# Kernel tuning notes

Hardware: AMD Instinct MI355X
Metric: run time of the kernel (lower is better)

Reference implementation:

```python
import math
import jax, jax.numpy as jnp
import numpy as np

B, W_LEN, C = 4, 2048, 768
H = 3  # fixed number of heads in the module
K = C // H  # head dim


def setup_inputs() -> dict:
    key = jax.random.key(0)
    k1, k2, k3 = jax.random.split(key, 3)
    in_sequence_bwc = jax.random.normal(k1, (B, W_LEN, C), dtype=jnp.float32)
    # torch nn.Linear weights: [out_features, in_features], scaled for stability
    W_qkv = jax.random.normal(k2, (3 * C, C), dtype=jnp.float32) * (1.0 / math.sqrt(C))
    W_proj = jax.random.normal(k3, (C, C), dtype=jnp.float32) * (1.0 / math.sqrt(C))
    return {"in_sequence_bwc": in_sequence_bwc, "W_qkv": W_qkv, "W_proj": W_proj}


def reference(in_sequence_bwc, W_qkv, W_proj):
    batch, words, coords = in_sequence_bwc.shape
    head_dim = coords // H
    # qkv projection: x @ W^T  -> [b, w, 3c]
    all_bwd = jnp.einsum("bwc,dc->bwd", in_sequence_bwc, W_qkv)
    q_bwc, k_bwc, v_bwc = jnp.split(all_bwd, 3, axis=-1)
    # [b, h, w, k]
    q = q_bwc.reshape(batch, words, H, head_dim).transpose(0, 2, 1, 3)
    k = k_bwc.reshape(batch, words, H, head_dim).transpose(0, 2, 1, 3)
    v = v_bwc.reshape(batch, words, H, head_dim).transpose(0, 2, 1, 3)
    # scaled scores with causal mask -> softmax -> @V
    scores = jnp.einsum("bhqk,bhmk->bhqm", q, k) / math.sqrt(head_dim)
    causal = jnp.tril(jnp.ones((words, words), dtype=bool))
    scores = jnp.where(causal[None, None], scores, -jnp.inf)
    probs = jax.nn.softmax(scores, axis=-1)
    out = jnp.einsum("bhqm,bhmk->bhqk", probs, v)
    out_bwc = out.transpose(0, 2, 1, 3).reshape(batch, words, coords)
    return jnp.einsum("bwc,dc->bwd", out_bwc, W_proj)
```

## Files before the change

### kernel.cpp

```cpp
#include <hip/hip_runtime.h>

using v8h = __attribute__((ext_vector_type(8))) _Float16;
using v4f = __attribute__((ext_vector_type(4))) float;
using v4u = __attribute__((ext_vector_type(4))) unsigned short;
using v8u = __attribute__((ext_vector_type(8))) unsigned short;

__device__ __forceinline__ unsigned short f2h(float x) {
  _Float16 h = (_Float16)x;
  return __builtin_bit_cast(unsigned short, h);
}
__device__ __forceinline__ float h2f(unsigned short u) {
  return (float)__builtin_bit_cast(_Float16, u);
}

__device__ __forceinline__ void gl_lds16(const unsigned short* g, unsigned short* l) {
  __builtin_amdgcn_global_load_lds(
      (const __attribute__((address_space(1))) unsigned int*)g,
      (__attribute__((address_space(3))) unsigned int*)l, 16, 0, 0);
}

__global__ void cvt3_kernel(const float* __restrict__ X,
                            const float* __restrict__ Wq,
                            const float* __restrict__ Wp,
                            unsigned short* __restrict__ Xb,
                            unsigned short* __restrict__ Wqb,
                            unsigned short* __restrict__ Wpb) {
  const int blk = (int)blockIdx.x;
  const float* src;
  unsigned short* dst;
  int i;
  if (blk < 3072)      { src = X;  dst = Xb;  i = blk * 256 + threadIdx.x; }
  else if (blk < 3936) { src = Wq; dst = Wqb; i = (blk - 3072) * 256 + threadIdx.x; }
  else                 { src = Wp; dst = Wpb; i = (blk - 3936) * 256 + threadIdx.x; }
  const float* p = src + (size_t)i * 8;
  float4 a = *(const float4*)p;
  float4 b = *(const float4*)(p + 4);
  v8u o = {f2h(a.x), f2h(a.y), f2h(a.z), f2h(a.w),
           f2h(b.x), f2h(b.y), f2h(b.z), f2h(b.w)};
  *(v8u*)(dst + (size_t)i * 8) = o;
}

template <int OMODE>
__global__ __launch_bounds__(512, 2)
void gemm8_kernel(const unsigned short* __restrict__ A,
                  const unsigned short* __restrict__ Bw,
                  void* __restrict__ Cout) {
  __shared__ unsigned short sm[65536];
  const int t    = (int)threadIdx.x;
  const int ln   = t & 63;
  const int wv   = t >> 6;
  const int quad = ln >> 4;
  const int L    = ln & 15;
  const int wm   = wv >> 2;
  const int wn   = wv & 3;
  const long m0  = (long)blockIdx.y * 256;
  const long n0  = (long)blockIdx.x * 256;

  const int srow = t >> 3;
  const int scol = ((t & 7) ^ (srow & 7)) * 8;
  const unsigned short* Ath = A + (m0 + srow) * 768 + scol;
  const unsigned short* Bth = Bw + (n0 + srow) * 768 + scol;
  unsigned short* lth = &sm[t * 8];

  const int l7   = L & 7;
  const int sl0  = ((0 + quad) ^ l7) * 8;
  const int sl1  = ((4 + quad) ^ l7) * 8;
  const int arow = (wm * 128 + L) * 64;
  const int brow = (wn * 64 + L) * 64;

  v4f acc[8][4];
#pragma unroll
  for (int i = 0; i < 8; i++)
#pragma unroll
    for (int j = 0; j < 4; j++) acc[i][j] = (v4f){0.f, 0.f, 0.f, 0.f};

  auto stA = [&](int tile, int h) {
    if (tile >= 12) return;
    const unsigned short* g = Ath + (h * 128) * 768 + tile * 64;
    unsigned short* l = lth + (tile & 1) * 32768 + h * 8192;
    gl_lds16(g, l);
    gl_lds16(g + 64 * 768, l + 4096);
  };
  auto stB = [&](int tile, int h) {
    if (tile >= 12) return;
    const unsigned short* g = Bth + (h * 128) * 768 + tile * 64;
    unsigned short* l = lth + (tile & 1) * 32768 + 16384 + h * 8192;
    gl_lds16(g, l);
    gl_lds16(g + 64 * 768, l + 4096);
  };

  stB(0, 0); stB(0, 1); stA(0, 0); stA(0, 1);
  stB(1, 0); stB(1, 1); stA(1, 0);
  asm volatile("s_waitcnt vmcnt(6)" ::: "memory");
  __builtin_amdgcn_s_barrier();
  __builtin_amdgcn_sched_barrier(0);

#pragma unroll 2
  for (int kt = 0; kt < 12; ++kt) {
    const unsigned short* sA = &sm[(kt & 1) * 32768];
    const unsigned short* sB = sA + 16384;
    v8h af[4][2], b0[2][2], b1[2][2];

#pragma unroll
    for (int i = 0; i < 4; i++) {
      af[i][0] = *(const v8h*)&sA[arow + i * 1024 + sl0];
      af[i][1] = *(const v8h*)&sA[arow + i * 1024 + sl1];
    }
#pragma unroll
    for (int j = 0; j < 2; j++) {
      b0[j][0] = *(const v8h*)&sB[brow + j * 1024 + sl0];
      b0[j][1] = *(const v8h*)&sB[brow + j * 1024 + sl1];
    }
    stA(kt + 1, 1);
    __builtin_amdgcn_s_barrier();
    asm volatile("s_waitcnt lgkmcnt(0)" ::: "memory");
    __builtin_amdgcn_sched_barrier(0);
    __builtin_amdgcn_s_setprio(1);
#pragma unroll
    for (int i = 0; i < 4; i++)
#pragma unroll
      for (int j = 0; j < 2; j++) {
        acc[i][j] = __builtin_amdgcn_mfma_f32_16x16x32_f16(af[i][0], b0[j][0], acc[i][j], 0, 0, 0);
        acc[i][j] = __builtin_amdgcn_mfma_f32_16x16x32_f16(af[i][1], b0[j][1], acc[i][j], 0, 0, 0);
      }
    __builtin_amdgcn_s_setprio(0);
    __builtin_amdgcn_s_barrier();
    __builtin_amdgcn_sched_barrier(0);

#pragma unroll
    for (int j = 0; j < 2; j++) {
      b1[j][0] = *(const v8h*)&sB[brow + 2048 + j * 1024 + sl0];
      b1[j][1] = *(const v8h*)&sB[brow + 2048 + j * 1024 + sl1];
    }
    __builtin_amdgcn_s_barrier();
    asm volatile("s_waitcnt lgkmcnt(0)" ::: "memory");
    __builtin_amdgcn_sched_barrier(0);
    __builtin_amdgcn_s_setprio(1);
#pragma unroll
    for (int i = 0; i < 4; i++)
#pragma unroll
      for (int j = 0; j < 2; j++) {
        acc[i][2 + j] = __builtin_amdgcn_mfma_f32_16x16x32_f16(af[i][0], b1[j][0], acc[i][2 + j], 0, 0, 0);
        acc[i][2 + j] = __builtin_amdgcn_mfma_f32_16x16x32_f16(af[i][1], b1[j][1], acc[i][2 + j], 0, 0, 0);
      }
    __builtin_amdgcn_s_setprio(0);
    __builtin_amdgcn_s_barrier();
    __builtin_amdgcn_sched_barrier(0);

#pragma unroll
    for (int i = 0; i < 4; i++) {
      af[i][0] = *(const v8h*)&sA[arow + 4096 + i * 1024 + sl0];
      af[i][1] = *(const v8h*)&sA[arow + 4096 + i * 1024 + sl1];
    }
    stB(kt + 2, 0);
    __builtin_amdgcn_s_barrier();
    asm volatile("s_waitcnt lgkmcnt(0)" ::: "memory");
    __builtin_amdgcn_sched_barrier(0);
    __builtin_amdgcn_s_setprio(1);
#pragma unroll
    for (int i = 0; i < 4; i++)
#pragma unroll
      for (int j = 0; j < 2; j++) {
        acc[4 + i][2 + j] = __builtin_amdgcn_mfma_f32_16x16x32_f16(af[i][0], b1[j][0], acc[4 + i][2 + j], 0, 0, 0);
        acc[4 + i][2 + j] = __builtin_amdgcn_mfma_f32_16x16x32_f16(af[i][1], b1[j][1], acc[4 + i][2 + j], 0, 0, 0);
      }
    __builtin_amdgcn_s_setprio(0);
    __builtin_amdgcn_s_barrier();
    __builtin_amdgcn_sched_barrier(0);

    stB(kt + 2, 1);
    stA(kt + 2, 0);
    __builtin_amdgcn_s_barrier();
    __builtin_amdgcn_sched_barrier(0);
    __builtin_amdgcn_s_setprio(1);
#pragma unroll
    for (int i = 0; i < 4; i++)
#pragma unroll
      for (int j = 0; j < 2; j++) {
        acc[4 + i][j] = __builtin_amdgcn_mfma_f32_16x16x32_f16(af[i][0], b0[j][0], acc[4 + i][j], 0, 0, 0);
        acc[4 + i][j] = __builtin_amdgcn_mfma_f32_16x16x32_f16(af[i][1], b0[j][1], acc[4 + i][j], 0, 0, 0);
      }
    __builtin_amdgcn_s_setprio(0);
    if (kt + 2 < 12)      { asm volatile("s_waitcnt vmcnt(6)" ::: "memory"); }
    else if (kt + 1 < 12) { asm volatile("s_waitcnt vmcnt(0)" ::: "memory"); }
    __builtin_amdgcn_s_barrier();
    __builtin_amdgcn_sched_barrier(0);
  }

#pragma unroll
  for (int mi = 0; mi < 8; mi++) {
    const long row = m0 + wm * 128 + (mi >> 2) * 64 + (mi & 3) * 16 + quad * 4;
#pragma unroll
    for (int nj = 0; nj < 4; nj++) {
      const long col = n0 + wn * 64 + nj * 16 + L;
#pragma unroll
      for (int r = 0; r < 4; r++) {
        if (OMODE == 0)
          ((unsigned short*)Cout)[(row + r) * 1536 + col] = f2h(acc[mi][nj][r]);
        else
          ((float*)Cout)[(row + r) * 768 + col] = acc[mi][nj][r];
      }
    }
  }
}

__global__ __launch_bounds__(512, 2)
void scv8_kernel(const unsigned short* __restrict__ QK,
                 const unsigned short* __restrict__ Xb,
                 const unsigned short* __restrict__ Wq,
                 unsigned short* __restrict__ Sc,
                 unsigned short* __restrict__ VT) {
  __shared__ unsigned short sm[65536];
  const int t    = (int)threadIdx.x;
  const int ln   = t & 63;
  const int wv   = t >> 6;
  const int quad = ln >> 4;
  const int L    = ln & 15;
  const int wm   = wv >> 2;
  const int wn   = wv & 3;

  const int x = (int)blockIdx.x;
  const bool isV = (x < 96);
  int NT, Ihi = 0, Jhi = 0, bh = 0, mt = 0, nt = 0;
  const unsigned short* Abase;
  const unsigned short* Bbase;
  long astr, bstr;

  if (isV) {
    mt = x & 31;
    nt = x >> 5;
    Abase = Xb + (long)mt * 256 * 768;
    Bbase = Wq + (long)(1536 + nt * 256) * 768;
    astr = 768; bstr = 768; NT = 12;
  } else {
    int s = x - 96;
    bh = s / 36;
    int slot = s % 36;
    while (slot >= Ihi + 1) { slot -= Ihi + 1; Ihi++; }
    Jhi = slot;
    const int b = bh / 3, h = bh % 3;
    Abase = QK + ((long)b * 2048 + Ihi * 256) * 1536 + h * 256;
    Bbase = QK + ((long)b * 2048 + Jhi * 256) * 1536 + 768 + h * 256;
    astr = 1536; bstr = 1536; NT = 4;
  }

  const int srow = t >> 3;
  const int scol = ((t & 7) ^ (srow & 7)) * 8;
  const unsigned short* Ath = Abase + (long)srow * astr + scol;
  const unsigned short* Bth = Bbase + (long)srow * bstr + scol;
  unsigned short* lth = &sm[t * 8];

  const int l7   = L & 7;
  const int sl0  = ((0 + quad) ^ l7) * 8;
  const int sl1  = ((4 + quad) ^ l7) * 8;
  const int arow = (wm * 128 + L) * 64;
  const int brow = (wn * 64 + L) * 64;

  v4f acc[8][4];
#pragma unroll
  for (int i = 0; i < 8; i++)
#pragma unroll
    for (int j = 0; j < 4; j++) acc[i][j] = (v4f){0.f, 0.f, 0.f, 0.f};

  auto stA = [&](int tile, int h) {
    if (tile >= NT) return;
    const unsigned short* g = Ath + (long)(h * 128) * astr + tile * 64;
    unsigned short* l = lth + (tile & 1) * 32768 + h * 8192;
    gl_lds16(g, l);
    gl_lds16(g + 64 * astr, l + 4096);
  };
  auto stB = [&](int tile, int h) {
    if (tile >= NT) return;
    const unsigned short* g = Bth + (long)(h * 128) * bstr + tile * 64;
    unsigned short* l = lth + (tile & 1) * 32768 + 16384 + h * 8192;
    gl_lds16(g, l);
    gl_lds16(g + 64 * bstr, l + 4096);
  };

  stB(0, 0); stB(0, 1); stA(0, 0); stA(0, 1);
  stB(1, 0); stB(1, 1); stA(1, 0);
  asm volatile("s_waitcnt vmcnt(6)" ::: "memory");
  __builtin_amdgcn_s_barrier();
  __builtin_amdgcn_sched_barrier(0);

#pragma unroll 2
  for (int kt = 0; kt < NT; ++kt) {
    const unsigned short* sA = &sm[(kt & 1) * 32768];
    const unsigned short* sB = sA + 16384;
    v8h af[4][2], b0[2][2], b1[2][2];

#pragma unroll
    for (int i = 0; i < 4; i++) {
      af[i][0] = *(const v8h*)&sA[arow + i * 1024 + sl0];
      af[i][1] = *(const v8h*)&sA[arow + i * 1024 + sl1];
    }
#pragma unroll
    for (int j = 0; j < 2; j++) {
      b0[j][0] = *(const v8h*)&sB[brow + j * 1024 + sl0];
      b0[j][1] = *(const v8h*)&sB[brow + j * 1024 + sl1];
    }
    stA(kt + 1, 1);
    __builtin_amdgcn_s_barrier();
    asm volatile("s_waitcnt lgkmcnt(0)" ::: "memory");
    __builtin_amdgcn_sched_barrier(0);
    __builtin_amdgcn_s_setprio(1);
#pragma unroll
    for (int i = 0; i < 4; i++)
#pragma unroll
      for (int j = 0; j < 2; j++) {
        acc[i][j] = __builtin_amdgcn_mfma_f32_16x16x32_f16(af[i][0], b0[j][0], acc[i][j], 0, 0, 0);
        acc[i][j] = __builtin_amdgcn_mfma_f32_16x16x32_f16(af[i][1], b0[j][1], acc[i][j], 0, 0, 0);
      }
    __builtin_amdgcn_s_setprio(0);
    __builtin_amdgcn_s_barrier();
    __builtin_amdgcn_sched_barrier(0);

#pragma unroll
    for (int j = 0; j < 2; j++) {
      b1[j][0] = *(const v8h*)&sB[brow + 2048 + j * 1024 + sl0];
      b1[j][1] = *(const v8h*)&sB[brow + 2048 + j * 1024 + sl1];
    }
    __builtin_amdgcn_s_barrier();
    asm volatile("s_waitcnt lgkmcnt(0)" ::: "memory");
    __builtin_amdgcn_sched_barrier(0);
    __builtin_amdgcn_s_setprio(1);
#pragma unroll
    for (int i = 0; i < 4; i++)
#pragma unroll
      for (int j = 0; j < 2; j++) {
        acc[i][2 + j] = __builtin_amdgcn_mfma_f32_16x16x32_f16(af[i][0], b1[j][0], acc[i][2 + j], 0, 0, 0);
        acc[i][2 + j] = __builtin_amdgcn_mfma_f32_16x16x32_f16(af[i][1], b1[j][1], acc[i][2 + j], 0, 0, 0);
      }
    __builtin_amdgcn_s_setprio(0);
    __builtin_amdgcn_s_barrier();
    __builtin_amdgcn_sched_barrier(0);

#pragma unroll
    for (int i = 0; i < 4; i++) {
      af[i][0] = *(const v8h*)&sA[arow + 4096 + i * 1024 + sl0];
      af[i][1] = *(const v8h*)&sA[arow + 4096 + i * 1024 + sl1];
    }
    stB(kt + 2, 0);
    __builtin_amdgcn_s_barrier();
    asm volatile("s_waitcnt lgkmcnt(0)" ::: "memory");
    __builtin_amdgcn_sched_barrier(0);
    __builtin_amdgcn_s_setprio(1);
#pragma unroll
    for (int i = 0; i < 4; i++)
#pragma unroll
      for (int j = 0; j < 2; j++) {
        acc[4 + i][2 + j] = __builtin_amdgcn_mfma_f32_16x16x32_f16(af[i][0], b1[j][0], acc[4 + i][2 + j], 0, 0, 0);
        acc[4 + i][2 + j] = __builtin_amdgcn_mfma_f32_16x16x32_f16(af[i][1], b1[j][1], acc[4 + i][2 + j], 0, 0, 0);
      }
    __builtin_amdgcn_s_setprio(0);
    __builtin_amdgcn_s_barrier();
    __builtin_amdgcn_sched_barrier(0);

    stB(kt + 2, 1);
    stA(kt + 2, 0);
    __builtin_amdgcn_s_barrier();
    __builtin_amdgcn_sched_barrier(0);
    __builtin_amdgcn_s_setprio(1);
#pragma unroll
    for (int i = 0; i < 4; i++)
#pragma unroll
      for (int j = 0; j < 2; j++) {
        acc[4 + i][j] = __builtin_amdgcn_mfma_f32_16x16x32_f16(af[i][0], b0[j][0], acc[4 + i][j], 0, 0, 0);
        acc[4 + i][j] = __builtin_amdgcn_mfma_f32_16x16x32_f16(af[i][1], b0[j][1], acc[4 + i][j], 0, 0, 0);
      }
    __builtin_amdgcn_s_setprio(0);
    if (kt + 2 < NT)      { asm volatile("s_waitcnt vmcnt(6)" ::: "memory"); }
    else if (kt + 1 < NT) { asm volatile("s_waitcnt vmcnt(0)" ::: "memory"); }
    __builtin_amdgcn_s_barrier();
    __builtin_amdgcn_sched_barrier(0);
  }

  if (isV) {
#pragma unroll
    for (int mi = 0; mi < 8; mi++) {
      const long token = (long)mt * 256 + wm * 128 + (mi >> 2) * 64 + (mi & 3) * 16 + quad * 4;
      const int b  = (int)(token >> 11);
      const int tk = (int)(token & 2047);
#pragma unroll
      for (int nj = 0; nj < 4; nj++) {
        const int colp = nt * 256 + wn * 64 + nj * 16 + L;
        const int h    = colp >> 8;
        const int d    = colp & 255;
        v4u val = {f2h(acc[mi][nj][0]), f2h(acc[mi][nj][1]),
                   f2h(acc[mi][nj][2]), f2h(acc[mi][nj][3])};
        *(v4u*)(&VT[((long)(b * 3 + h) * 256 + d) * 2048 + tk]) = val;
      }
    }
  } else {
    const int di = wm;
    const int dj = wn >> 1;
    const int i128 = 2 * Ihi + di;
    const int j128 = 2 * Jhi + dj;
    if (j128 <= i128) {
      unsigned short* Sb = Sc + ((long)bh * 136 + (long)i128 * (i128 + 1) / 2 + j128) * 16384;
#pragma unroll
      for (int mi = 0; mi < 8; mi++) {
        const int subrow = (mi >> 2) * 64 + (mi & 3) * 16 + quad * 4;
#pragma unroll
        for (int nj = 0; nj < 4; nj++) {
          const int subcol = (wn & 1) * 64 + nj * 16 + L;
#pragma unroll
          for (int r = 0; r < 4; r++)
            Sb[(subrow + r) * 128 + subcol] = f2h(acc[mi][nj][r]);
        }
      }
    }
  }
}

__global__ __launch_bounds__(512, 1)
void pvf_kernel(const unsigned short* __restrict__ Sc,
                const unsigned short* __restrict__ VT,
                unsigned short* __restrict__ AO) {
  __shared__ unsigned short sm[36864];
  __shared__ float fbuf[128];

  const int t    = (int)threadIdx.x;
  const int ln   = t & 63;
  const int wv   = t >> 6;
  const int quad = ln >> 4;
  const int L    = ln & 15;

  const int p  = (int)blockIdx.x >> 1;
  const int nh = (int)blockIdx.x & 1;
  const int bh = (int)blockIdx.y;
  const int b  = bh / 3, h = bh % 3;

  const unsigned short* VTb = VT + ((long)(bh * 256 + nh * 128)) * 2048;
  const int rloc = wv * 16 + L;

  auto stageV = [&](int jj, unsigned short* base) {
#pragma unroll
    for (int pp = 0; pp < 4; pp++) {
      const int sidx = pp * 512 + t;
      const int d    = sidx >> 4;
      const int ph   = sidx & 15;
      gl_lds16(VTb + (long)d * 2048 + jj * 128 + ((ph ^ (d & 7)) * 8),
               base + sidx * 8);
    }
  };

  for (int sel = 0; sel < 2; ++sel) {
    const int i = sel ? (15 - p) : p;
    const long Sbase = ((long)bh * 136 + (long)i * (i + 1) / 2) * 16384;

    v4f acc[8];
#pragma unroll
    for (int n = 0; n < 8; n++) acc[n] = (v4f){0.f, 0.f, 0.f, 0.f};
    float m_run = -1e30f, l_run = 0.f;

    v8u s_cur[4], s_nxt[4];
    {
      const unsigned short* Sp = Sc + Sbase + (long)rloc * 128;
#pragma unroll
      for (int ks = 0; ks < 4; ks++)
        s_cur[ks] = *(const v8u*)(Sp + ks * 32 + quad * 8);
      __builtin_amdgcn_sched_barrier(0);
      stageV(0, &sm[0]);
      __builtin_amdgcn_sched_barrier(0);
    }

    for (int j = 0; j <= i; ++j) {
      const int jn = (j < i) ? (j + 1) : i;
      const bool clamped = (j == i);
      {
        const unsigned short* Sp = Sc + Sbase + (long)jn * 16384 + (long)rloc * 128;
#pragma unroll
        for (int ks = 0; ks < 4; ks++)
          s_nxt[ks] = *(const v8u*)(Sp + ks * 32 + quad * 8);
      }
      __builtin_amdgcn_sched_barrier(0);
      if (clamped) {
#pragma unroll
        for (int pp = 0; pp < 4; pp++) {
          const int sidx = pp * 512 + t;
          const int d    = sidx >> 4;
          const int ph   = sidx & 15;
          gl_lds16(VTb + (long)d * 2048 + jn * 128 + ((ph ^ (d & 7)) * 8),
                   &sm[32768 + t * 8]);
        }
      } else {
        stageV(jn, &sm[(jn & 1) * 16384]);
      }
      __builtin_amdgcn_sched_barrier(0);

      float pv[4][8];
      float mx = -1e30f;
      if (j == i) {
#pragma unroll
        for (int ks = 0; ks < 4; ks++)
#pragma unroll
          for (int e = 0; e < 8; e++) {
            const bool valid = (ks * 32 + quad * 8 + e) <= rloc;
            const float f = valid ? h2f(s_cur[ks][e]) * 0.0625f : -1e30f;
            pv[ks][e] = f;
            mx = fmaxf(mx, f);
          }
      } else {
#pragma unroll
        for (int ks = 0; ks < 4; ks++)
#pragma unroll
          for (int e = 0; e < 8; e++) {
            const float f = h2f(s_cur[ks][e]) * 0.0625f;
            pv[ks][e] = f;
            mx = fmaxf(mx, f);
          }
      }
      mx = fmaxf(mx, __shfl_xor(mx, 16));
      mx = fmaxf(mx, __shfl_xor(mx, 32));
      const float m_new = fmaxf(m_run, mx);
      const float alpha = __expf(m_run - m_new);
      m_run = m_new;

      float sum = 0.f;
      v8h pa[4];
#pragma unroll
      for (int ks = 0; ks < 4; ks++) {
        v8h ph16;
#pragma unroll
        for (int e = 0; e < 8; e++) {
          const float pe = __expf(pv[ks][e] - m_new);
          sum += pe;
          ph16[e] = (_Float16)pe;
        }
        pa[ks] = ph16;
      }
      sum += __shfl_xor(sum, 16);
      sum += __shfl_xor(sum, 32);
      l_run = l_run * alpha + sum;

      if (quad == 0) fbuf[wv * 16 + L] = alpha;
      asm volatile("s_waitcnt lgkmcnt(0)" ::: "memory");
      __builtin_amdgcn_sched_barrier(0);
      const float a0 = fbuf[wv * 16 + quad * 4 + 0];
      const float a1 = fbuf[wv * 16 + quad * 4 + 1];
      const float a2 = fbuf[wv * 16 + quad * 4 + 2];
      const float a3 = fbuf[wv * 16 + quad * 4 + 3];
#pragma unroll
      for (int n = 0; n < 8; n++) {
        acc[n][0] *= a0; acc[n][1] *= a1; acc[n][2] *= a2; acc[n][3] *= a3;
      }

      asm volatile("s_waitcnt vmcnt(8)" ::: "memory");
      __builtin_amdgcn_s_barrier();
      __builtin_amdgcn_sched_barrier(0);

      const unsigned short* vb = &sm[(j & 1) * 16384];
      const int dx = L & 7;
#pragma unroll
      for (int nfc = 0; nfc < 8; nfc++) {
        const int dbase = (nfc * 16 + L) * 128;
        v8h v0 = *(const v8h*)&vb[dbase + ((0 + quad) ^ dx) * 8];
        v8h v1 = *(const v8h*)&vb[dbase + ((4 + quad) ^ dx) * 8];
        v8h v2 = *(const v8h*)&vb[dbase + ((8 + quad) ^ dx) * 8];
        v8h v3 = *(const v8h*)&vb[dbase + ((12 + quad) ^ dx) * 8];
        acc[nfc] = __builtin_amdgcn_mfma_f32_16x16x32_f16(pa[0], v0, acc[nfc], 0, 0, 0);
        acc[nfc] = __builtin_amdgcn_mfma_f32_16x16x32_f16(pa[1], v1, acc[nfc], 0, 0, 0);
        acc[nfc] = __builtin_amdgcn_mfma_f32_16x16x32_f16(pa[2], v2, acc[nfc], 0, 0, 0);
        acc[nfc] = __builtin_amdgcn_mfma_f32_16x16x32_f16(pa[3], v3, acc[nfc], 0, 0, 0);
      }
      __builtin_amdgcn_s_barrier();
      __builtin_amdgcn_sched_barrier(0);

#pragma unroll
      for (int ks = 0; ks < 4; ks++) s_cur[ks] = s_nxt[ks];
    }

    const float inv = 1.0f / l_run;
    if (quad == 0) fbuf[wv * 16 + L] = inv;
    asm volatile("s_waitcnt lgkmcnt(0)" ::: "memory");
    __builtin_amdgcn_sched_barrier(0);
    const float i0 = fbuf[wv * 16 + quad * 4 + 0];
    const float i1 = fbuf[wv * 16 + quad * 4 + 1];
    const float i2 = fbuf[wv * 16 + quad * 4 + 2];
    const float i3 = fbuf[wv * 16 + quad * 4 + 3];

    unsigned short* Ob = AO + ((long)b * 2048 + (long)i * 128 + wv * 16 + quad * 4) * 768
                            + h * 256 + nh * 128 + L;
#pragma unroll
    for (int n = 0; n < 8; n++) {
      Ob[0 * 768 + n * 16] = f2h(acc[n][0] * i0);
      Ob[1 * 768 + n * 16] = f2h(acc[n][1] * i1);
      Ob[2 * 768 + n * 16] = f2h(acc[n][2] * i2);
      Ob[3 * 768 + n * 16] = f2h(acc[n][3] * i3);
    }
    __builtin_amdgcn_s_barrier();
  }
}

extern "C" void kernel_launch(void* const* d_in, const int* in_sizes, int n_in,
                              void* d_out, int out_size, void* d_ws, size_t ws_size,
                              hipStream_t stream) {
  const float* X     = (const float*)d_in[0];
  const float* Wqkv  = (const float*)d_in[1];
  const float* Wproj = (const float*)d_in[2];
  float* out = (float*)d_out;

  const size_t SZ_QK = (size_t)8192 * 1536 * 2;
  const size_t SZ_VT = (size_t)3072 * 2048 * 2;
  const size_t SZ_SC = (size_t)12 * 136 * 16384 * 2;
  const size_t SZ_AO = (size_t)8192 * 768 * 2;
  const size_t SZ_WQ = (size_t)2304 * 768 * 2;

  char* ws = (char*)d_ws;
  unsigned short* QKb = (unsigned short*)ws;
  unsigned short* VTb = (unsigned short*)(ws + SZ_QK);
  unsigned short* Scb = (unsigned short*)(ws + SZ_QK + SZ_VT);
  unsigned short* AOb = (unsigned short*)(ws + SZ_QK + SZ_VT + SZ_SC);
  unsigned short* Xb  = AOb;
  unsigned short* Wqb = (unsigned short*)(ws + SZ_QK + SZ_VT + SZ_SC + SZ_AO);
  unsigned short* Wpb = (unsigned short*)(ws + SZ_QK + SZ_VT + SZ_SC + SZ_AO + SZ_WQ);

  dim3 blk(256, 1, 1);
  cvt3_kernel<<<dim3(4224, 1, 1), blk, 0, stream>>>(X, Wqkv, Wproj, Xb, Wqb, Wpb);
  gemm8_kernel<0><<<dim3(6, 32, 1), dim3(512, 1, 1), 0, stream>>>(Xb, Wqb, QKb);
  scv8_kernel<<<dim3(528, 1, 1), dim3(512, 1, 1), 0, stream>>>(QKb, Xb, Wqb, Scb, VTb);
  pvf_kernel<<<dim3(16, 12, 1), dim3(512, 1, 1), 0, stream>>>(Scb, VTb, AOb);
  gemm8_kernel<1><<<dim3(3, 32, 1), dim3(512, 1, 1), 0, stream>>>(AOb, Wpb, out);
}
```

Measured before the change: 227.6 us.

## Load V fragments directly from global into registers in PV kernel

Drops the LDS double-buffered staging of the V tile, the swizzled gl_lds loads and both workgroup barriers per iteration in the PV kernel. Each lane now loads its V fragments straight from global/L2 into registers. The softmax probabilities are recomputed from the raw scores instead of being kept in a float array. The aim is to cut barrier syncs and LDS traffic, at the cost of redundant global reads across the 8 waves, higher register pressure, and exposed load latency because the V loads are no longer prefetched one step ahead.

```diff
diff --git a/kernel.cpp b/kernel.cpp
--- a/kernel.cpp
+++ b/kernel.cpp
@@ -417,7 +417,6 @@
 void pvf_kernel(const unsigned short* __restrict__ Sc,
                 const unsigned short* __restrict__ VT,
                 unsigned short* __restrict__ AO) {
-  __shared__ unsigned short sm[36864];
   __shared__ float fbuf[128];
 
   const int t    = (int)threadIdx.x;
@@ -434,16 +433,7 @@
   const unsigned short* VTb = VT + ((long)(bh * 256 + nh * 128)) * 2048;
   const int rloc = wv * 16 + L;
 
-  auto stageV = [&](int jj, unsigned short* base) {
-#pragma unroll
-    for (int pp = 0; pp < 4; pp++) {
-      const int sidx = pp * 512 + t;
-      const int d    = sidx >> 4;
-      const int ph   = sidx & 15;
-      gl_lds16(VTb + (long)d * 2048 + jj * 128 + ((ph ^ (d & 7)) * 8),
-               base + sidx * 8);
-    }
-  };
+  const unsigned short* Vl = VTb + (long)L * 2048 + quad * 8;
 
   for (int sel = 0; sel < 2; ++sel) {
     const int i = sel ? (15 - p) : p;
@@ -460,36 +450,23 @@
 #pragma unroll
       for (int ks = 0; ks < 4; ks++)
         s_cur[ks] = *(const v8u*)(Sp + ks * 32 + quad * 8);
-      __builtin_amdgcn_sched_barrier(0);
-      stageV(0, &sm[0]);
-      __builtin_amdgcn_sched_barrier(0);
     }
 
     for (int j = 0; j <= i; ++j) {
       const int jn = (j < i) ? (j + 1) : i;
-      const bool clamped = (j == i);
       {
         const unsigned short* Sp = Sc + Sbase + (long)jn * 16384 + (long)rloc * 128;
 #pragma unroll
         for (int ks = 0; ks < 4; ks++)
           s_nxt[ks] = *(const v8u*)(Sp + ks * 32 + quad * 8);
       }
-      __builtin_amdgcn_sched_barrier(0);
-      if (clamped) {
-#pragma unroll
-        for (int pp = 0; pp < 4; pp++) {
-          const int sidx = pp * 512 + t;
-          const int d    = sidx >> 4;
-          const int ph   = sidx & 15;
-          gl_lds16(VTb + (long)d * 2048 + jn * 128 + ((ph ^ (d & 7)) * 8),
-                   &sm[32768 + t * 8]);
-        }
-      } else {
-        stageV(jn, &sm[(jn & 1) * 16384]);
-      }
-      __builtin_amdgcn_sched_barrier(0);
-
-      float pv[4][8];
+      v8h vf[4][8];
+#pragma unroll
+      for (int ks = 0; ks < 4; ks++)
+#pragma unroll
+        for (int nfc = 0; nfc < 8; nfc++)
+          vf[ks][nfc] = *(const v8h*)(Vl + (long)nfc * 32768 + j * 128 + ks * 32);
+
       float mx = -1e30f;
       if (j == i) {
 #pragma unroll
@@ -498,18 +475,14 @@
           for (int e = 0; e < 8; e++) {
             const bool valid = (ks * 32 + quad * 8 + e) <= rloc;
             const float f = valid ? h2f(s_cur[ks][e]) * 0.0625f : -1e30f;
-            pv[ks][e] = f;
             mx = fmaxf(mx, f);
           }
       } else {
 #pragma unroll
         for (int ks = 0; ks < 4; ks++)
 #pragma unroll
-          for (int e = 0; e < 8; e++) {
-            const float f = h2f(s_cur[ks][e]) * 0.0625f;
-            pv[ks][e] = f;
-            mx = fmaxf(mx, f);
-          }
+          for (int e = 0; e < 8; e++)
+            mx = fmaxf(mx, h2f(s_cur[ks][e]) * 0.0625f);
       }
       mx = fmaxf(mx, __shfl_xor(mx, 16));
       mx = fmaxf(mx, __shfl_xor(mx, 32));
@@ -519,16 +492,32 @@
 
       float sum = 0.f;
       v8h pa[4];
-#pragma unroll
-      for (int ks = 0; ks < 4; ks++) {
-        v8h ph16;
-#pragma unroll
-        for (int e = 0; e < 8; e++) {
-          const float pe = __expf(pv[ks][e] - m_new);
-          sum += pe;
-          ph16[e] = (_Float16)pe;
+      if (j == i) {
+#pragma unroll
+        for (int ks = 0; ks < 4; ks++) {
+          v8h ph16;
+#pragma unroll
+          for (int e = 0; e < 8; e++) {
+            const bool valid = (ks * 32 + quad * 8 + e) <= rloc;
+            const float f = valid ? h2f(s_cur[ks][e]) * 0.0625f : -1e30f;
+            const float pe = __expf(f - m_new);
+            sum += pe;
+            ph16[e] = (_Float16)pe;
+          }
+          pa[ks] = ph16;
         }
-        pa[ks] = ph16;
+      } else {
+#pragma unroll
+        for (int ks = 0; ks < 4; ks++) {
+          v8h ph16;
+#pragma unroll
+          for (int e = 0; e < 8; e++) {
+            const float pe = __expf(h2f(s_cur[ks][e]) * 0.0625f - m_new);
+            sum += pe;
+            ph16[e] = (_Float16)pe;
+          }
+          pa[ks] = ph16;
+        }
       }
       sum += __shfl_xor(sum, 16);
       sum += __shfl_xor(sum, 32);
@@ -541,31 +530,20 @@
       const float a1 = fbuf[wv * 16 + quad * 4 + 1];
       const float a2 = fbuf[wv * 16 + quad * 4 + 2];
       const float a3 = fbuf[wv * 16 + quad * 4 + 3];
+      asm volatile("s_waitcnt lgkmcnt(0)" ::: "memory");
+      __builtin_amdgcn_sched_barrier(0);
 #pragma unroll
       for (int n = 0; n < 8; n++) {
         acc[n][0] *= a0; acc[n][1] *= a1; acc[n][2] *= a2; acc[n][3] *= a3;
       }
 
-      asm volatile("s_waitcnt vmcnt(8)" ::: "memory");
-      __builtin_amdgcn_s_barrier();
-      __builtin_amdgcn_sched_barrier(0);
-
-      const unsigned short* vb = &sm[(j & 1) * 16384];
-      const int dx = L & 7;
 #pragma unroll
       for (int nfc = 0; nfc < 8; nfc++) {
-        const int dbase = (nfc * 16 + L) * 128;
-        v8h v0 = *(const v8h*)&vb[dbase + ((0 + quad) ^ dx) * 8];
-        v8h v1 = *(const v8h*)&vb[dbase + ((4 + quad) ^ dx) * 8];
-        v8h v2 = *(const v8h*)&vb[dbase + ((8 + quad) ^ dx) * 8];
-        v8h v3 = *(const v8h*)&vb[dbase + ((12 + quad) ^ dx) * 8];
-        acc[nfc] = __builtin_amdgcn_mfma_f32_16x16x32_f16(pa[0], v0, acc[nfc], 0, 0, 0);
-        acc[nfc] = __builtin_amdgcn_mfma_f32_16x16x32_f16(pa[1], v1, acc[nfc], 0, 0, 0);
-        acc[nfc] = __builtin_amdgcn_mfma_f32_16x16x32_f16(pa[2], v2, acc[nfc], 0, 0, 0);
-        acc[nfc] = __builtin_amdgcn_mfma_f32_16x16x32_f16(pa[3], v3, acc[nfc], 0, 0, 0);
-      }
-      __builtin_amdgcn_s_barrier();
-      __builtin_amdgcn_sched_barrier(0);
+        acc[nfc] = __builtin_amdgcn_mfma_f32_16x16x32_f16(pa[0], vf[0][nfc], acc[nfc], 0, 0, 0);
+        acc[nfc] = __builtin_amdgcn_mfma_f32_16x16x32_f16(pa[1], vf[1][nfc], acc[nfc], 0, 0, 0);
+        acc[nfc] = __builtin_amdgcn_mfma_f32_16x16x32_f16(pa[2], vf[2][nfc], acc[nfc], 0, 0, 0);
+        acc[nfc] = __builtin_amdgcn_mfma_f32_16x16x32_f16(pa[3], vf[3][nfc], acc[nfc], 0, 0, 0);
+      }
 
 #pragma unroll
       for (int ks = 0; ks < 4; ks++) s_cur[ks] = s_nxt[ks];
@@ -579,6 +557,8 @@
     const float i1 = fbuf[wv * 16 + quad * 4 + 1];
     const float i2 = fbuf[wv * 16 + quad * 4 + 2];
     const float i3 = fbuf[wv * 16 + quad * 4 + 3];
+    asm volatile("s_waitcnt lgkmcnt(0)" ::: "memory");
+    __builtin_amdgcn_sched_barrier(0);
 
     unsigned short* Ob = AO + ((long)b * 2048 + (long)i * 128 + wv * 16 + quad * 4) * 768
                             + h * 256 + nh * 128 + L;
@@ -589,7 +569,6 @@
       Ob[2 * 768 + n * 16] = f2h(acc[n][2] * i2);
       Ob[3 * 768 + n * 16] = f2h(acc[n][3] * i3);
     }
-    __builtin_amdgcn_s_barrier();
   }
 }
 
```

New measurement: 317.9 us. 1.4x slower.

## Split paired causal row tiles into separate blocks and raise PV kernel occupancy

Applied to the files above, without the earlier changes.

The PV/softmax kernel previously processed two complementary causal row tiles per block. Each block now handles a single row tile, with the grid doubled and longest tiles scheduled first, so more CUs get work. Launch bounds now target four blocks per CU, and the LDS buffer drops the extra clamp slot by skipping the prefetch on the last iteration. The tighter register budget may cause spills, and per-block load balance is left to the hardware scheduler.

```diff
diff --git a/kernel.cpp b/kernel.cpp
--- a/kernel.cpp
+++ b/kernel.cpp
@@ -413,11 +413,11 @@
   }
 }
 
-__global__ __launch_bounds__(512, 1)
+__global__ __launch_bounds__(512, 4)
 void pvf_kernel(const unsigned short* __restrict__ Sc,
                 const unsigned short* __restrict__ VT,
                 unsigned short* __restrict__ AO) {
-  __shared__ unsigned short sm[36864];
+  __shared__ unsigned short sm[32768];
   __shared__ float fbuf[128];
 
   const int t    = (int)threadIdx.x;
@@ -426,8 +426,9 @@
   const int quad = ln >> 4;
   const int L    = ln & 15;
 
-  const int p  = (int)blockIdx.x >> 1;
-  const int nh = (int)blockIdx.x & 1;
+  const int x  = (int)blockIdx.x;
+  const int i  = 15 - (x >> 1);
+  const int nh = x & 1;
   const int bh = (int)blockIdx.y;
   const int b  = bh / 3, h = bh % 3;
 
@@ -445,151 +446,136 @@
     }
   };
 
-  for (int sel = 0; sel < 2; ++sel) {
-    const int i = sel ? (15 - p) : p;
-    const long Sbase = ((long)bh * 136 + (long)i * (i + 1) / 2) * 16384;
-
-    v4f acc[8];
-#pragma unroll
-    for (int n = 0; n < 8; n++) acc[n] = (v4f){0.f, 0.f, 0.f, 0.f};
-    float m_run = -1e30f, l_run = 0.f;
-
-    v8u s_cur[4], s_nxt[4];
-    {
-      const unsigned short* Sp = Sc + Sbase + (long)rloc * 128;
+  const long Sbase = ((long)bh * 136 + (long)i * (i + 1) / 2) * 16384;
+
+  v4f acc[8];
+#pragma unroll
+  for (int n = 0; n < 8; n++) acc[n] = (v4f){0.f, 0.f, 0.f, 0.f};
+  float m_run = -1e30f, l_run = 0.f;
+
+  v8u s_cur[4], s_nxt[4];
+  {
+    const unsigned short* Sp = Sc + Sbase + (long)rloc * 128;
+#pragma unroll
+    for (int ks = 0; ks < 4; ks++)
+      s_cur[ks] = *(const v8u*)(Sp + ks * 32 + quad * 8);
+    __builtin_amdgcn_sched_barrier(0);
+    stageV(0, &sm[0]);
+    __builtin_amdgcn_sched_barrier(0);
+  }
+
+  for (int j = 0; j <= i; ++j) {
+    const bool last = (j == i);
+    if (!last) {
+      const unsigned short* Sp = Sc + Sbase + (long)(j + 1) * 16384 + (long)rloc * 128;
 #pragma unroll
       for (int ks = 0; ks < 4; ks++)
-        s_cur[ks] = *(const v8u*)(Sp + ks * 32 + quad * 8);
+        s_nxt[ks] = *(const v8u*)(Sp + ks * 32 + quad * 8);
       __builtin_amdgcn_sched_barrier(0);
-      stageV(0, &sm[0]);
+      stageV(j + 1, &sm[((j + 1) & 1) * 16384]);
       __builtin_amdgcn_sched_barrier(0);
     }
 
-    for (int j = 0; j <= i; ++j) {
-      const int jn = (j < i) ? (j + 1) : i;
-      const bool clamped = (j == i);
-      {
-        const unsigned short* Sp = Sc + Sbase + (long)jn * 16384 + (long)rloc * 128;
-#pragma unroll
-        for (int ks = 0; ks < 4; ks++)
-          s_nxt[ks] = *(const v8u*)(Sp + ks * 32 + quad * 8);
-      }
-      __builtin_amdgcn_sched_barrier(0);
-      if (clamped) {
-#pragma unroll
-        for (int pp = 0; pp < 4; pp++) {
-          const int sidx = pp * 512 + t;
-          const int d    = sidx >> 4;
-          const int ph   = sidx & 15;
-          gl_lds16(VTb + (long)d * 2048 + jn * 128 + ((ph ^ (d & 7)) * 8),
-                   &sm[32768 + t * 8]);
+    float pv[4][8];
+    float mx = -1e30f;
+    if (last) {
+#pragma unroll
+      for (int ks = 0; ks < 4; ks++)
+#pragma unroll
+        for (int e = 0; e < 8; e++) {
+          const bool valid = (ks * 32 + quad * 8 + e) <= rloc;
+          const float f = valid ? h2f(s_cur[ks][e]) * 0.0625f : -1e30f;
+          pv[ks][e] = f;
+          mx = fmaxf(mx, f);
         }
-      } else {
-        stageV(jn, &sm[(jn & 1) * 16384]);
-      }
-      __builtin_amdgcn_sched_barrier(0);
-
-      float pv[4][8];
-      float mx = -1e30f;
-      if (j == i) {
-#pragma unroll
-        for (int ks = 0; ks < 4; ks++)
-#pragma unroll
-          for (int e = 0; e < 8; e++) {
-            const bool valid = (ks * 32 + quad * 8 + e) <= rloc;
-            const float f = valid ? h2f(s_cur[ks][e]) * 0.0625f : -1e30f;
-            pv[ks][e] = f;
-            mx = fmaxf(mx, f);
-          }
-      } else {
-#pragma unroll
-        for (int ks = 0; ks < 4; ks++)
-#pragma unroll
-          for (int e = 0; e < 8; e++) {
-            const float f = h2f(s_cur[ks][e]) * 0.0625f;
-            pv[ks][e] = f;
-            mx = fmaxf(mx, f);
-          }
-      }
-      mx = fmaxf(mx, __shfl_xor(mx, 16));
-      mx = fmaxf(mx, __shfl_xor(mx, 32));
-      const float m_new = fmaxf(m_run, mx);
-      const float alpha = __expf(m_run - m_new);
-      m_run = m_new;
-
-      float sum = 0.f;
-      v8h pa[4];
-#pragma unroll
-      for (int ks = 0; ks < 4; ks++) {
-        v8h ph16;
+    } else {
+#pragma unroll
+      for (int ks = 0; ks < 4; ks++)
 #pragma unroll
         for (int e = 0; e < 8; e++) {
-          const float pe = __expf(pv[ks][e] - m_new);
-          sum += pe;
-          ph16[e] = (_Float16)pe;
+          const float f = h2f(s_cur[ks][e]) * 0.0625f;
+          pv[ks][e] = f;
+          mx = fmaxf(mx, f);
         }
-        pa[ks] = ph16;
-      }
-      sum += __shfl_xor(sum, 16);
-      sum += __shfl_xor(sum, 32);
-      l_run = l_run * alpha + sum;
-
-      if (quad == 0) fbuf[wv * 16 + L] = alpha;
-      asm volatile("s_waitcnt lgkmcnt(0)" ::: "memory");
-      __builtin_amdgcn_sched_barrier(0);
-      const float a0 = fbuf[wv * 16 + quad * 4 + 0];
-      const float a1 = fbuf[wv * 16 + quad * 4 + 1];
-      const float a2 = fbuf[wv * 16 + quad * 4 + 2];
-      const float a3 = fbuf[wv * 16 + quad * 4 + 3];
-#pragma unroll
-      for (int n = 0; n < 8; n++) {
-        acc[n][0] *= a0; acc[n][1] *= a1; acc[n][2] *= a2; acc[n][3] *= a3;
-      }
-
-      asm volatile("s_waitcnt vmcnt(8)" ::: "memory");
-      __builtin_amdgcn_s_barrier();
-      __builtin_amdgcn_sched_barrier(0);
-
-      const unsigned short* vb = &sm[(j & 1) * 16384];
-      const int dx = L & 7;
-#pragma unroll
-      for (int nfc = 0; nfc < 8; nfc++) {
-        const int dbase = (nfc * 16 + L) * 128;
-        v8h v0 = *(const v8h*)&vb[dbase + ((0 + quad) ^ dx) * 8];
-        v8h v1 = *(const v8h*)&vb[dbase + ((4 + quad) ^ dx) * 8];
-        v8h v2 = *(const v8h*)&vb[dbase + ((8 + quad) ^ dx) * 8];
-        v8h v3 = *(const v8h*)&vb[dbase + ((12 + quad) ^ dx) * 8];
-        acc[nfc] = __builtin_amdgcn_mfma_f32_16x16x32_f16(pa[0], v0, acc[nfc], 0, 0, 0);
-        acc[nfc] = __builtin_amdgcn_mfma_f32_16x16x32_f16(pa[1], v1, acc[nfc], 0, 0, 0);
-        acc[nfc] = __builtin_amdgcn_mfma_f32_16x16x32_f16(pa[2], v2, acc[nfc], 0, 0, 0);
-        acc[nfc] = __builtin_amdgcn_mfma_f32_16x16x32_f16(pa[3], v3, acc[nfc], 0, 0, 0);
-      }
-      __builtin_amdgcn_s_barrier();
-      __builtin_amdgcn_sched_barrier(0);
-
-#pragma unroll
-      for (int ks = 0; ks < 4; ks++) s_cur[ks] = s_nxt[ks];
-    }
-
-    const float inv = 1.0f / l_run;
-    if (quad == 0) fbuf[wv * 16 + L] = inv;
+    }
+    mx = fmaxf(mx, __shfl_xor(mx, 16));
+    mx = fmaxf(mx, __shfl_xor(mx, 32));
+    const float m_new = fmaxf(m_run, mx);
+    const float alpha = __expf(m_run - m_new);
+    m_run = m_new;
+
+    float sum = 0.f;
+    v8h pa[4];
+#pragma unroll
+    for (int ks = 0; ks < 4; ks++) {
+      v8h ph16;
+#pragma unroll
+      for (int e = 0; e < 8; e++) {
+        const float pe = __expf(pv[ks][e] - m_new);
+        sum += pe;
+        ph16[e] = (_Float16)pe;
+      }
+      pa[ks] = ph16;
+    }
+    sum += __shfl_xor(sum, 16);
+    sum += __shfl_xor(sum, 32);
+    l_run = l_run * alpha + sum;
+
+    if (quad == 0) fbuf[wv * 16 + L] = alpha;
     asm volatile("s_waitcnt lgkmcnt(0)" ::: "memory");
     __builtin_amdgcn_sched_barrier(0);
-    const float i0 = fbuf[wv * 16 + quad * 4 + 0];
-    const float i1 = fbuf[wv * 16 + quad * 4 + 1];
-    const float i2 = fbuf[wv * 16 + quad * 4 + 2];
-    const float i3 = fbuf[wv * 16 + quad * 4 + 3];
-
-    unsigned short* Ob = AO + ((long)b * 2048 + (long)i * 128 + wv * 16 + quad * 4) * 768
-                            + h * 256 + nh * 128 + L;
+    const float a0 = fbuf[wv * 16 + quad * 4 + 0];
+    const float a1 = fbuf[wv * 16 + quad * 4 + 1];
+    const float a2 = fbuf[wv * 16 + quad * 4 + 2];
+    const float a3 = fbuf[wv * 16 + quad * 4 + 3];
 #pragma unroll
     for (int n = 0; n < 8; n++) {
-      Ob[0 * 768 + n * 16] = f2h(acc[n][0] * i0);
-      Ob[1 * 768 + n * 16] = f2h(acc[n][1] * i1);
-      Ob[2 * 768 + n * 16] = f2h(acc[n][2] * i2);
-      Ob[3 * 768 + n * 16] = f2h(acc[n][3] * i3);
-    }
-    __builtin_amdgcn_s_barrier();
+      acc[n][0] *= a0; acc[n][1] *= a1; acc[n][2] *= a2; acc[n][3] *= a3;
+    }
+
+    if (!last) { asm volatile("s_waitcnt vmcnt(8)" ::: "memory"); }
+    else       { asm volatile("s_waitcnt vmcnt(0)" ::: "memory"); }
+    __builtin_amdgcn_s_barrier();
+    __builtin_amdgcn_sched_barrier(0);
+
+    const unsigned short* vb = &sm[(j & 1) * 16384];
+    const int dx = L & 7;
+#pragma unroll
+    for (int nfc = 0; nfc < 8; nfc++) {
+      const int dbase = (nfc * 16 + L) * 128;
+      v8h v0 = *(const v8h*)&vb[dbase + ((0 + quad) ^ dx) * 8];
+      v8h v1 = *(const v8h*)&vb[dbase + ((4 + quad) ^ dx) * 8];
+      v8h v2 = *(const v8h*)&vb[dbase + ((8 + quad) ^ dx) * 8];
+      v8h v3 = *(const v8h*)&vb[dbase + ((12 + quad) ^ dx) * 8];
+      acc[nfc] = __builtin_amdgcn_mfma_f32_16x16x32_f16(pa[0], v0, acc[nfc], 0, 0, 0);
+      acc[nfc] = __builtin_amdgcn_mfma_f32_16x16x32_f16(pa[1], v1, acc[nfc], 0, 0, 0);
+      acc[nfc] = __builtin_amdgcn_mfma_f32_16x16x32_f16(pa[2], v2, acc[nfc], 0, 0, 0);
+      acc[nfc] = __builtin_amdgcn_mfma_f32_16x16x32_f16(pa[3], v3, acc[nfc], 0, 0, 0);
+    }
+    __builtin_amdgcn_s_barrier();
+    __builtin_amdgcn_sched_barrier(0);
+
+#pragma unroll
+    for (int ks = 0; ks < 4; ks++) s_cur[ks] = s_nxt[ks];
+  }
+
+  const float inv = 1.0f / l_run;
+  if (quad == 0) fbuf[wv * 16 + L] = inv;
+  asm volatile("s_waitcnt lgkmcnt(0)" ::: "memory");
+  __builtin_amdgcn_sched_barrier(0);
+  const float i0 = fbuf[wv * 16 + quad * 4 + 0];
+  const float i1 = fbuf[wv * 16 + quad * 4 + 1];
+  const float i2 = fbuf[wv * 16 + quad * 4 + 2];
+  const float i3 = fbuf[wv * 16 + quad * 4 + 3];
+
+  unsigned short* Ob = AO + ((long)b * 2048 + (long)i * 128 + wv * 16 + quad * 4) * 768
+                          + h * 256 + nh * 128 + L;
+#pragma unroll
+  for (int n = 0; n < 8; n++) {
+    Ob[0 * 768 + n * 16] = f2h(acc[n][0] * i0);
+    Ob[1 * 768 + n * 16] = f2h(acc[n][1] * i1);
+    Ob[2 * 768 + n * 16] = f2h(acc[n][2] * i2);
+    Ob[3 * 768 + n * 16] = f2h(acc[n][3] * i3);
   }
 }
 
@@ -620,6 +606,6 @@
   cvt3_kernel<<<dim3(4224, 1, 1), blk, 0, stream>>>(X, Wqkv, Wproj, Xb, Wqb, Wpb);
   gemm8_kernel<0><<<dim3(6, 32, 1), dim3(512, 1, 1), 0, stream>>>(Xb, Wqb, QKb);
   scv8_kernel<<<dim3(528, 1, 1), dim3(512, 1, 1), 0, stream>>>(QKb, Xb, Wqb, Scb, VTb);
-  pvf_kernel<<<dim3(16, 12, 1), dim3(512, 1, 1), 0, stream>>>(Scb, VTb, AOb);
+  pvf_kernel<<<dim3(32, 12, 1), dim3(512, 1, 1), 0, stream>>>(Scb, VTb, AOb);
   gemm8_kernel<1><<<dim3(3, 32, 1), dim3(512, 1, 1), 0, stream>>>(AOb, Wpb, out);
 }
```

After: 248.9 us. +9.3%, slower.
